# Performance work log

Hardware: AMD Instinct MI355X
Metric: run time of the kernel (lower is better)

## Reference

```python
import jax, jax.numpy as jnp
import numpy as np

EPS_DIST = 1e-10
BN_EPS = 1e-5
K = 3  # nsample / three_nn


def setup_inputs() -> dict:
    key = jax.random.key(0)
    ks = jax.random.split(key, 8)
    B, N, S, D1, D2 = 4, 8192, 2048, 128, 256
    C_in = D1 + D2  # 384
    H = 256
    inp = {
        "pos1": jax.random.normal(ks[0], (B, 3, N), dtype=jnp.float32),
        "pos2": jax.random.normal(ks[1], (B, 3, S), dtype=jnp.float32),
        "feature1": jax.random.normal(ks[2], (B, D1, N), dtype=jnp.float32),
        "feature2": jax.random.normal(ks[3], (B, D2, S), dtype=jnp.float32),
        # MLP layer 1: Conv1d(384->256, k=1) + BN
        "W1": jax.random.normal(ks[4], (H, C_in), dtype=jnp.float32) * (1.0 / np.sqrt(C_in)),
        "b1": jnp.zeros((H,), dtype=jnp.float32),
        "g1": jnp.ones((H,), dtype=jnp.float32),
        "be1": jnp.zeros((H,), dtype=jnp.float32),
        # MLP layer 2: Conv1d(256->256, k=1) + BN
        "W2": jax.random.normal(ks[5], (H, H), dtype=jnp.float32) * (1.0 / np.sqrt(H)),
        "b2": jnp.zeros((H,), dtype=jnp.float32),
        "g2": jnp.ones((H,), dtype=jnp.float32),
        "be2": jnp.zeros((H,), dtype=jnp.float32),
    }
    return inp


def _conv_bn_relu(x, W, b, gamma, beta):
    # x: [B, Cin, N]; 1x1 Conv1d == channel GEMM
    y = jnp.einsum("oc,bcn->bon", W, x) + b[None, :, None]
    # BatchNorm1d in training mode: batch statistics over (B, N)
    mean = jnp.mean(y, axis=(0, 2), keepdims=True)
    var = jnp.mean(jnp.square(y - mean), axis=(0, 2), keepdims=True)
    y = (y - mean) * jax.lax.rsqrt(var + BN_EPS)
    y = y * gamma[None, :, None] + beta[None, :, None]
    return jax.nn.relu(y)


def reference(pos1, pos2, feature1, feature2, W1, b1, g1, be1, W2, b2, g2, be2):
    # pos1: [B,3,N], pos2: [B,3,S], feature1: [B,D1,N], feature2: [B,D2,S]
    p1 = jnp.swapaxes(pos1, 1, 2)  # [B,N,3]
    p2 = jnp.swapaxes(pos2, 1, 2)  # [B,S,3]
    # three_nn: squared-distance 3-NN of each point in p1 among p2
    d2 = (jnp.sum(p1 * p1, -1)[:, :, None]
          + jnp.sum(p2 * p2, -1)[:, None, :]
          - 2.0 * jnp.einsum("bnc,bsc->bns", p1, p2))  # [B,N,S]
    neg_vals, idx = jax.lax.top_k(-d2, K)  # idx: [B,N,3]
    dists = jnp.maximum(-neg_vals, EPS_DIST)  # dists[dists<1e-10]=1e-10
    w = 1.0 / dists
    w = w / jnp.sum(w, -1, keepdims=True)  # [B,N,3]
    # grouping_operation: gather feature2 [B,D,S] by idx -> [B,D,N,3]
    grouped = jax.vmap(lambda f, i: f[:, i])(feature2, idx)
    interpolated = jnp.sum(grouped * w[:, None, :, :], axis=-1)  # [B,D2,N]
    feat = jnp.concatenate([interpolated, feature1], axis=1)  # [B,384,N]
    feat = _conv_bn_relu(feat, W1, b1, g1, be1)
    feat = _conv_bn_relu(feat, W2, b2, g2, be2)
    return feat  # [B,256,N]
```

## Files before the change

### kernel.cpp

```cpp
#include <hip/hip_runtime.h>
#include <hip/hip_bf16.h>
#include <cstdint>

typedef unsigned short u16;
typedef unsigned int u32;
typedef unsigned long long u64;
typedef __bf16 bf16x8 __attribute__((ext_vector_type(8)));
typedef float f32x4 __attribute__((ext_vector_type(4)));
typedef u16 u16x8 __attribute__((ext_vector_type(8)));

__device__ __forceinline__ u16 f2b(float f) {
    unsigned int u = __float_as_uint(f);
    u += 0x7fffu + ((u >> 16) & 1u);
    return (u16)(u >> 16);
}
__device__ __forceinline__ float b2f(u16 h) {
    return __uint_as_float(((unsigned int)h) << 16);
}
__device__ __forceinline__ void async_cp16(void* lds, const void* g) {
    __builtin_amdgcn_global_load_lds((const __attribute__((address_space(1))) void*)g,
                                     (__attribute__((address_space(3))) void*)lds, 16, 0, 0);
}
__device__ __forceinline__ u32 fmono(float f) {
    u32 u = __float_as_uint(f);
    return u ^ (((u32)((int)u >> 31)) | 0x80000000u);
}
__device__ __forceinline__ u64 shfl_xor_u64(u64 v, int mask) {
    u32 lo = (u32)v, hi = (u32)(v >> 32);
    lo = (u32)__shfl_xor((int)lo, mask);
    hi = (u32)__shfl_xor((int)hi, mask);
    return ((u64)hi << 32) | lo;
}
__device__ __forceinline__ void ins3(u64 k, u64& k0, u64& k1, u64& k2) {
    bool c0 = k > k0, c1 = k > k1, c2 = k > k2;
    k2 = c1 ? k1 : (c2 ? k : k2);
    k1 = c0 ? k0 : (c1 ? k : k1);
    k0 = c0 ? k : k0;
}
__device__ __forceinline__ int pkix(int i) { return i + (i >> 6); }

#define NB_NN  1024
#define NB_CVT 160
#define NB_T2  512
#define NB_T1  1024

__global__ __launch_bounds__(256, 8) void prep_kernel(const float* __restrict__ w1,
                                                      const float* __restrict__ w2,
                                                      u16* __restrict__ wb,
                                                      const float* __restrict__ feature2,
                                                      u16* __restrict__ f2t,
                                                      const float* __restrict__ feature1,
                                                      u16* __restrict__ f1t,
                                                      const float* __restrict__ pos1,
                                                      const float* __restrict__ pos2,
                                                      int* __restrict__ idx_out,
                                                      float* __restrict__ w_out) {
    __shared__ __align__(16) char smem[19712];
    int bi = blockIdx.x;
    int tid = threadIdx.x;

    if (bi >= NB_NN) {
        int ci = bi - NB_NN;
        if (ci < NB_CVT) {
            int i = ci * 256 + tid;
            if (i < 40960) {
                const float* src = (i < 24576) ? w1 : w2;
                int k = (i < 24576) ? i : (i - 24576);
                float4 v = *(const float4*)&src[(size_t)k * 4];
                ushort4 o;
                o.x = f2b(v.x); o.y = f2b(v.y); o.z = f2b(v.z); o.w = f2b(v.w);
                *(ushort4*)&wb[(size_t)i * 4] = o;
            }
            return;
        }
        float (*t)[65] = (float (*)[65])smem;
        const float* in; u16* out; int C, S, s0, c0, b;
        if (ci < NB_CVT + NB_T2) {
            int lin = ci - NB_CVT;
            C = 256; S = 2048; in = feature2; out = f2t;
            s0 = (lin & 31) * 64; c0 = ((lin >> 5) & 3) * 64; b = lin >> 7;
        } else {
            int lin = ci - NB_CVT - NB_T2;
            C = 128; S = 8192; in = feature1; out = f1t;
            s0 = (lin & 127) * 64; c0 = ((lin >> 7) & 1) * 64; b = lin >> 8;
        }
        const float* ib = in + (size_t)b * C * S;
        u16* ob = out + (size_t)b * S * C;
        int col = tid & 63, r0 = tid >> 6;
#pragma unroll
        for (int p = 0; p < 16; ++p) {
            int c = p * 4 + r0;
            t[c][col] = ib[(size_t)(c0 + c) * S + s0 + col];
        }
        __syncthreads();
#pragma unroll
        for (int p = 0; p < 16; ++p) {
            int s = p * 4 + r0;
            ob[(size_t)(s0 + s) * C + c0 + col] = f2b(t[col][s]);
        }
        return;
    }

    float4* pk = (float4*)smem;
    u64* warr = (u64*)(smem + 16640);
    int j0 = bi * 32;
    int b = j0 >> 13;
    const float* p2 = pos2 + (size_t)b * 3 * 2048;
    int p = tid & 15, ck = tid >> 4;
    int wv = tid >> 6, lane = tid & 63;
    int na = (j0 & 8191) + p, nbq = na + 16;
    const float* p1 = pos1 + (size_t)b * 3 * 8192;
    float xa = p1[na], ya = p1[8192 + na], za = p1[16384 + na];
    float xb = p1[nbq], yb = p1[8192 + nbq], zb = p1[16384 + nbq];

    u64 a0k = 0, a1k = 0, a2k = 0, b0k = 0, b1k = 0, b2k = 0;

    for (int half = 0; half < 2; ++half) {
        int hbase = half * 1024;
        for (int i = tid; i < 1024; i += 256) {
            int s = hbase + i;
            float x = p2[s], y = p2[2048 + s], z = p2[4096 + s];
            pk[pkix(i)] = make_float4(x, y, z, -0.5f * (x * x + y * y + z * z));
        }
        __syncthreads();

        float ga0 = -3.4e38f, ga1 = -3.4e38f, ga2 = -3.4e38f;
        float gb0 = -3.4e38f, gb1 = -3.4e38f, gb2 = -3.4e38f;
        int ia0 = 0, ia1 = 0, ia2 = 0, ib0 = 0, ib1 = 0, ib2 = 0;
        int sb = ck * 64;
        const float4* pc = pk + pkix(sb);
#pragma unroll 4
        for (int it = 0; it < 64; ++it) {
            float4 cd = pc[it];
            int s = sb + it;
            float ta = fmaf(xa, cd.x, fmaf(ya, cd.y, fmaf(za, cd.z, cd.w)));
            float tb = fmaf(xb, cd.x, fmaf(yb, cd.y, fmaf(zb, cd.z, cd.w)));
            bool a0 = ta > ga0, a1 = ta > ga1, a2 = ta > ga2;
            ga2 = a1 ? ga1 : (a2 ? ta : ga2);
            ia2 = a1 ? ia1 : (a2 ? s : ia2);
            ga1 = a0 ? ga0 : (a1 ? ta : ga1);
            ia1 = a0 ? ia0 : (a1 ? s : ia1);
            ga0 = a0 ? ta : ga0;
            ia0 = a0 ? s : ia0;
            bool b0c = tb > gb0, b1c = tb > gb1, b2c = tb > gb2;
            gb2 = b1c ? gb1 : (b2c ? tb : gb2);
            ib2 = b1c ? ib1 : (b2c ? s : ib2);
            gb1 = b0c ? gb0 : (b1c ? tb : gb1);
            ib1 = b0c ? ib0 : (b1c ? s : ib1);
            gb0 = b0c ? tb : gb0;
            ib0 = b0c ? s : ib0;
        }
        __syncthreads();

        int gi0 = hbase + ia0, gi1 = hbase + ia1, gi2 = hbase + ia2;
        int gj0 = hbase + ib0, gj1 = hbase + ib1, gj2 = hbase + ib2;
        ins3(((u64)fmono(ga0) << 32) | (u64)(2047 - gi0), a0k, a1k, a2k);
        ins3(((u64)fmono(ga1) << 32) | (u64)(2047 - gi1), a0k, a1k, a2k);
        ins3(((u64)fmono(ga2) << 32) | (u64)(2047 - gi2), a0k, a1k, a2k);
        ins3(((u64)fmono(gb0) << 32) | (u64)(2047 - gj0), b0k, b1k, b2k);
        ins3(((u64)fmono(gb1) << 32) | (u64)(2047 - gj1), b0k, b1k, b2k);
        ins3(((u64)fmono(gb2) << 32) | (u64)(2047 - gj2), b0k, b1k, b2k);
    }

#pragma unroll
    for (int mask = 16; mask <= 32; mask <<= 1) {
        u64 pa0 = shfl_xor_u64(a0k, mask), pa1 = shfl_xor_u64(a1k, mask), pa2 = shfl_xor_u64(a2k, mask);
        u64 pb0 = shfl_xor_u64(b0k, mask), pb1 = shfl_xor_u64(b1k, mask), pb2 = shfl_xor_u64(b2k, mask);
        ins3(pa0, a0k, a1k, a2k); ins3(pa1, a0k, a1k, a2k); ins3(pa2, a0k, a1k, a2k);
        ins3(pb0, b0k, b1k, b2k); ins3(pb1, b0k, b1k, b2k); ins3(pb2, b0k, b1k, b2k);
    }
    if (lane < 16) {
        u64* wr = &warr[(wv * 16 + p) * 6];
        wr[0] = a0k; wr[1] = a1k; wr[2] = a2k;
        wr[3] = b0k; wr[4] = b1k; wr[5] = b2k;
    }
    __syncthreads();
    if (tid < 32) {
        int q = tid;
        int pp = q & 15, off = (q < 16) ? 0 : 3;
        const u64* w0 = &warr[pp * 6];
        u64 k0 = w0[off], k1 = w0[off + 1], k2 = w0[off + 2];
#pragma unroll
        for (int w = 1; w < 4; ++w) {
            const u64* wr = &warr[(w * 16 + pp) * 6];
            ins3(wr[off], k0, k1, k2);
            ins3(wr[off + 1], k0, k1, k2);
            ins3(wr[off + 2], k0, k1, k2);
        }
        int s0 = 2047 - (int)(k0 & 0xFFFFFFFFu);
        int s1 = 2047 - (int)(k1 & 0xFFFFFFFFu);
        int s2 = 2047 - (int)(k2 & 0xFFFFFFFFu);
        int j = j0 + q;
        int n = j & 8191;
        float x1 = p1[n], y1 = p1[8192 + n], z1 = p1[16384 + n];
        float n1 = x1 * x1 + y1 * y1 + z1 * z1;
        float X0 = p2[s0], Y0 = p2[2048 + s0], Z0 = p2[4096 + s0];
        float X1 = p2[s1], Y1v = p2[2048 + s1], Z1 = p2[4096 + s1];
        float X2 = p2[s2], Y2v = p2[2048 + s2], Z2 = p2[4096 + s2];
        float t0 = x1 * X0 + y1 * Y0 + z1 * Z0 - 0.5f * (X0 * X0 + Y0 * Y0 + Z0 * Z0);
        float t1 = x1 * X1 + y1 * Y1v + z1 * Z1 - 0.5f * (X1 * X1 + Y1v * Y1v + Z1 * Z1);
        float t2 = x1 * X2 + y1 * Y2v + z1 * Z2 - 0.5f * (X2 * X2 + Y2v * Y2v + Z2 * Z2);
        float d0 = fmaxf(fmaf(-2.f, t0, n1), 1e-10f);
        float d1 = fmaxf(fmaf(-2.f, t1, n1), 1e-10f);
        float d2 = fmaxf(fmaf(-2.f, t2, n1), 1e-10f);
        float w0v = 1.f / d0, w1v = 1.f / d1, w2v = 1.f / d2;
        float inv = 1.f / (w0v + w1v + w2v);
        idx_out[j * 3] = s0; idx_out[j * 3 + 1] = s1; idx_out[j * 3 + 2] = s2;
        w_out[j * 3] = w0v * inv; w_out[j * 3 + 1] = w1v * inv; w_out[j * 3 + 2] = w2v * inv;
    }
}

__global__ __launch_bounds__(256) void gather_kernel(const u16* __restrict__ f2t,
                                                     const int* __restrict__ idx,
                                                     const float* __restrict__ wgt,
                                                     u16* __restrict__ interp) {
    int wv = threadIdx.x >> 6, lane = threadIdx.x & 63;
    int j = blockIdx.x * 4 + wv;
    int b = j >> 13;
    int i0 = idx[j * 3], i1 = idx[j * 3 + 1], i2 = idx[j * 3 + 2];
    float w0 = wgt[j * 3], w1 = wgt[j * 3 + 1], w2 = wgt[j * 3 + 2];
    const u16* r0 = f2t + ((size_t)(b * 2048 + i0)) * 256;
    const u16* r1 = f2t + ((size_t)(b * 2048 + i1)) * 256;
    const u16* r2 = f2t + ((size_t)(b * 2048 + i2)) * 256;
    int c = lane * 4;
    ushort4 v0 = *(const ushort4*)(r0 + c);
    ushort4 v1 = *(const ushort4*)(r1 + c);
    ushort4 v2 = *(const ushort4*)(r2 + c);
    ushort4 o;
    o.x = f2b(w0 * b2f(v0.x) + w1 * b2f(v1.x) + w2 * b2f(v2.x));
    o.y = f2b(w0 * b2f(v0.y) + w1 * b2f(v1.y) + w2 * b2f(v2.y));
    o.z = f2b(w0 * b2f(v0.z) + w1 * b2f(v1.z) + w2 * b2f(v2.z));
    o.w = f2b(w0 * b2f(v0.w) + w1 * b2f(v1.w) + w2 * b2f(v2.w));
    *(ushort4*)(interp + (size_t)j * 256 + c) = o;
}

template <int KT, bool SPLIT, bool FUSE>
__global__ __launch_bounds__(256, 2) void gemm_kernel(const u16* __restrict__ A1,
                                                      const u16* __restrict__ A2,
                                                      const u16* __restrict__ Bw,
                                                      const float* __restrict__ bias,
                                                      const float* __restrict__ stats_in,
                                                      const float* __restrict__ g_in,
                                                      const float* __restrict__ be_in,
                                                      u16* __restrict__ Yb,
                                                      float* __restrict__ stats) {
    __shared__ __align__(16) char smemA[36864];
    u16* Al = (u16*)smemA;
    u16* Bl = (u16*)(smemA + 16384);
    u16* T  = (u16*)smemA;
    float2* BNT = (float2*)(smemA + 34816);
    int tid = threadIdx.x;
    int lane = tid & 63, wv = tid >> 6;
    int j0 = blockIdx.x * 128, m0 = blockIdx.y * 128;
    int l15 = lane & 15, q = lane >> 4;
    int wj = (wv >> 1) * 64, wm = (wv & 1) * 64;
    f32x4 acc[4][4];
#pragma unroll
    for (int i = 0; i < 4; ++i)
#pragma unroll
        for (int jj = 0; jj < 4; ++jj) acc[i][jj] = (f32x4){0.f, 0.f, 0.f, 0.f};

    if (FUSE) {
        int m = tid;
        const float inv = 1.f / 32768.f;
        float mean = stats_in[m] * inv;
        float var = stats_in[256 + m] * inv - mean * mean;
        float a = g_in[m] * rsqrtf(var + 1e-5f);
        BNT[m] = make_float2(a, be_in[m] - mean * a);
        __syncthreads();
    }

    int rbase = wv * 32;
    int lrow = lane >> 3, lchunk = lane & 7;
    const u16* Bg = Bw + (size_t)m0 * KT;

    for (int k0 = 0; k0 < KT; k0 += 64) {
        if (FUSE) {
            int c = k0 + lchunk * 8;
            float2 bn[8];
#pragma unroll
            for (int e = 0; e < 8; ++e) bn[e] = BNT[c + e];
#pragma unroll
            for (int qq = 0; qq < 4; ++qq) {
                int row = rbase + qq * 8;
                u16x8 y = *(const u16x8*)&A1[(size_t)(j0 + row + lrow) * 256 + c];
                u16x8 o;
#pragma unroll
                for (int e = 0; e < 8; ++e)
                    o[e] = f2b(fmaxf(b2f(y[e]) * bn[e].x + bn[e].y, 0.f));
                *(u16x8*)&Al[(row + lrow) * 64 + lchunk * 8] = o;
                async_cp16(&Bl[row * 64], Bg + (size_t)(row + lrow) * KT + k0 + lchunk * 8);
            }
        } else {
            const u16* src; int stride;
            if (!SPLIT || k0 < 256) { src = A1 + (size_t)j0 * 256 + k0; stride = 256; }
            else                    { src = A2 + (size_t)j0 * 128 + (k0 - 256); stride = 128; }
#pragma unroll
            for (int qq = 0; qq < 4; ++qq) {
                int row = rbase + qq * 8;
                async_cp16(&Al[row * 64], src + (size_t)(row + lrow) * stride + lchunk * 8);
                async_cp16(&Bl[row * 64], Bg + (size_t)(row + lrow) * KT + k0 + lchunk * 8);
            }
        }
        __syncthreads();
#pragma unroll
        for (int ks = 0; ks < 2; ++ks) {
            bf16x8 af[4], bfr[4];
#pragma unroll
            for (int i = 0; i < 4; ++i)
                af[i] = *(const bf16x8*)&Al[(wj + i * 16 + l15) * 64 + ks * 32 + q * 8];
#pragma unroll
            for (int i = 0; i < 4; ++i)
                bfr[i] = *(const bf16x8*)&Bl[(wm + i * 16 + l15) * 64 + ks * 32 + q * 8];
#pragma unroll
            for (int i = 0; i < 4; ++i)
#pragma unroll
                for (int jj = 0; jj < 4; ++jj)
                    acc[i][jj] = __builtin_amdgcn_mfma_f32_16x16x32_bf16(af[i], bfr[jj],
                                                                         acc[i][jj], 0, 0, 0);
        }
        __syncthreads();
    }
#pragma unroll
    for (int jj = 0; jj < 4; ++jj) {
        int ml = wm + jj * 16 + l15;
        float bv = bias[m0 + ml];
        float s = 0.f, s2 = 0.f;
#pragma unroll
        for (int i = 0; i < 4; ++i) {
            int jl = wj + i * 16 + q * 4;
#pragma unroll
            for (int r = 0; r < 4; ++r) {
                float v = acc[i][jj][r] + bv;
                s += v; s2 += v * v;
                T[(jl + r) * 136 + ml] = f2b(v);
            }
        }
        s += __shfl_xor(s, 16); s += __shfl_xor(s, 32);
        s2 += __shfl_xor(s2, 16); s2 += __shfl_xor(s2, 32);
        if (q == 0) {
            atomicAdd(&stats[m0 + ml], s);
            atomicAdd(&stats[256 + m0 + ml], s2);
        }
    }
    __syncthreads();
#pragma unroll
    for (int it = 0; it < 8; ++it) {
        int jl = it * 16 + wv * 4 + q;
        u16x8 v = *(const u16x8*)&T[jl * 136 + l15 * 8];
        *(u16x8*)&Yb[(size_t)(j0 + jl) * 256 + m0 + l15 * 8] = v;
    }
}

__global__ __launch_bounds__(256) void final_out_kernel(const u16* __restrict__ Y2,
                                                        const float* __restrict__ stats,
                                                        const float* __restrict__ g,
                                                        const float* __restrict__ be,
                                                        float* __restrict__ out) {
    __shared__ float t[64][65];
    int j0 = blockIdx.x * 64, o0 = blockIdx.y * 64;
    int tid = threadIdx.x;
    int c4 = (tid & 15) * 4, rw = tid >> 4;
#pragma unroll
    for (int p = 0; p < 4; ++p) {
        int jl = p * 16 + rw;
        ushort4 v = *(const ushort4*)&Y2[(size_t)(j0 + jl) * 256 + o0 + c4];
        t[jl][c4] = b2f(v.x); t[jl][c4 + 1] = b2f(v.y);
        t[jl][c4 + 2] = b2f(v.z); t[jl][c4 + 3] = b2f(v.w);
    }
    __syncthreads();
    int b = j0 >> 13, n0 = j0 & 8191;
    const float inv = 1.f / 32768.f;
#pragma unroll
    for (int p = 0; p < 4; ++p) {
        int ol = p * 16 + rw;
        int o = o0 + ol;
        float mean = stats[o] * inv;
        float var = stats[256 + o] * inv - mean * mean;
        float a = g[o] * rsqrtf(var + 1e-5f);
        float s = be[o] - mean * a;
        float4 v;
        v.x = fmaxf(t[c4][ol] * a + s, 0.f);
        v.y = fmaxf(t[c4 + 1][ol] * a + s, 0.f);
        v.z = fmaxf(t[c4 + 2][ol] * a + s, 0.f);
        v.w = fmaxf(t[c4 + 3][ol] * a + s, 0.f);
        *(float4*)&out[(size_t)b * 2097152 + (size_t)o * 8192 + n0 + c4] = v;
    }
}

extern "C" void kernel_launch(void* const* d_in, const int* in_sizes, int n_in,
                              void* d_out, int out_size, void* d_ws, size_t ws_size,
                              hipStream_t stream) {
    const float* pos1 = (const float*)d_in[0];
    const float* pos2 = (const float*)d_in[1];
    const float* feature1 = (const float*)d_in[2];
    const float* feature2 = (const float*)d_in[3];
    const float* W1 = (const float*)d_in[4];
    const float* b1 = (const float*)d_in[5];
    const float* g1 = (const float*)d_in[6];
    const float* be1 = (const float*)d_in[7];
    const float* W2 = (const float*)d_in[8];
    const float* b2 = (const float*)d_in[9];
    const float* g2 = (const float*)d_in[10];
    const float* be2 = (const float*)d_in[11];

    char* ws = (char*)d_ws;
    int*   IDX    = (int*)(ws + 0);
    float* WGT    = (float*)(ws + 393216);
    u16*   W1B    = (u16*)(ws + 786432);
    u16*   W2B    = (u16*)(ws + 983040);
    float* STATS  = (float*)(ws + 1114112);
    u16*   F2T    = (u16*)(ws + 1118208);
    u16*   F1T    = (u16*)(ws + 5312512);
    u16*   INTERP = (u16*)(ws + 13701120);
    u16*   Y1     = (u16*)(ws + 30478336);
    u16*   Y2     = (u16*)(ws + 47255552);
    float* OUT    = (float*)d_out;

    hipMemsetAsync(STATS, 0, 1024 * sizeof(float), stream);
    prep_kernel<<<NB_NN + NB_CVT + NB_T2 + NB_T1, 256, 0, stream>>>(
        W1, W2, W1B, feature2, F2T, feature1, F1T, pos1, pos2, IDX, WGT);
    gather_kernel<<<8192, 256, 0, stream>>>(F2T, IDX, WGT, INTERP);
    gemm_kernel<384, true, false><<<dim3(256, 2), 256, 0, stream>>>(
        INTERP, F1T, W1B, b1, nullptr, nullptr, nullptr, Y1, STATS);
    gemm_kernel<256, false, true><<<dim3(256, 2), 256, 0, stream>>>(
        Y1, nullptr, W2B, b2, STATS, g1, be1, Y2, STATS + 512);
    final_out_kernel<<<dim3(512, 4), 256, 0, stream>>>(Y2, STATS + 512, g2, be2, OUT);
}
```

Measured before the change: 201.9 us.

## Fuse 3-NN interpolation gather into first GEMM and widen NN blocks to 64 queries

Removes the separate gather kernel and the INTERP buffer. The first GEMM now builds its A tile for k<256 by loading the three neighbour rows of F2T, weighting and summing them, and writing the result to LDS directly. This saves a full write and reread of the interpolated activations, but the GEMM's A loads for those k-steps become synchronous and redundant across the two m-blocks. Separately, the three-NN search now handles 64 queries per block (4 per thread) instead of 32, which improves reuse of each pos2 LDS read. The cost is more registers, so launch bounds drop from 8 to 4 blocks.

```diff
diff --git a/kernel.cpp b/kernel.cpp
--- a/kernel.cpp
+++ b/kernel.cpp
@@ -39,12 +39,12 @@
 }
 __device__ __forceinline__ int pkix(int i) { return i + (i >> 6); }
 
-#define NB_NN  1024
+#define NB_NN  512
 #define NB_CVT 160
 #define NB_T2  512
 #define NB_T1  1024
 
-__global__ __launch_bounds__(256, 8) void prep_kernel(const float* __restrict__ w1,
+__global__ __launch_bounds__(256, 4) void prep_kernel(const float* __restrict__ w1,
                                                       const float* __restrict__ w2,
                                                       u16* __restrict__ wb,
                                                       const float* __restrict__ feature2,
@@ -55,7 +55,7 @@
                                                       const float* __restrict__ pos2,
                                                       int* __restrict__ idx_out,
                                                       float* __restrict__ w_out) {
-    __shared__ __align__(16) char smem[19712];
+    __shared__ __align__(16) char smem[22784];
     int bi = blockIdx.x;
     int tid = threadIdx.x;
 
@@ -103,17 +103,21 @@
 
     float4* pk = (float4*)smem;
     u64* warr = (u64*)(smem + 16640);
-    int j0 = bi * 32;
+    int j0 = bi * 64;
     int b = j0 >> 13;
     const float* p2 = pos2 + (size_t)b * 3 * 2048;
     int p = tid & 15, ck = tid >> 4;
     int wv = tid >> 6, lane = tid & 63;
-    int na = (j0 & 8191) + p, nbq = na + 16;
     const float* p1 = pos1 + (size_t)b * 3 * 8192;
-    float xa = p1[na], ya = p1[8192 + na], za = p1[16384 + na];
-    float xb = p1[nbq], yb = p1[8192 + nbq], zb = p1[16384 + nbq];
-
-    u64 a0k = 0, a1k = 0, a2k = 0, b0k = 0, b1k = 0, b2k = 0;
+    float qx[4], qy[4], qz[4];
+#pragma unroll
+    for (int t = 0; t < 4; ++t) {
+        int n = (j0 & 8191) + p + t * 16;
+        qx[t] = p1[n]; qy[t] = p1[8192 + n]; qz[t] = p1[16384 + n];
+    }
+    u64 key[4][3];
+#pragma unroll
+    for (int t = 0; t < 4; ++t) { key[t][0] = 0; key[t][1] = 0; key[t][2] = 0; }
 
     for (int half = 0; half < 2; ++half) {
         int hbase = half * 1024;
@@ -124,73 +128,76 @@
         }
         __syncthreads();
 
-        float ga0 = -3.4e38f, ga1 = -3.4e38f, ga2 = -3.4e38f;
-        float gb0 = -3.4e38f, gb1 = -3.4e38f, gb2 = -3.4e38f;
-        int ia0 = 0, ia1 = 0, ia2 = 0, ib0 = 0, ib1 = 0, ib2 = 0;
+        float g[4][3]; int id[4][3];
+#pragma unroll
+        for (int t = 0; t < 4; ++t) {
+            g[t][0] = -3.4e38f; g[t][1] = -3.4e38f; g[t][2] = -3.4e38f;
+            id[t][0] = 0; id[t][1] = 0; id[t][2] = 0;
+        }
         int sb = ck * 64;
         const float4* pc = pk + pkix(sb);
-#pragma unroll 4
+#pragma unroll 2
         for (int it = 0; it < 64; ++it) {
             float4 cd = pc[it];
             int s = sb + it;
-            float ta = fmaf(xa, cd.x, fmaf(ya, cd.y, fmaf(za, cd.z, cd.w)));
-            float tb = fmaf(xb, cd.x, fmaf(yb, cd.y, fmaf(zb, cd.z, cd.w)));
-            bool a0 = ta > ga0, a1 = ta > ga1, a2 = ta > ga2;
-            ga2 = a1 ? ga1 : (a2 ? ta : ga2);
-            ia2 = a1 ? ia1 : (a2 ? s : ia2);
-            ga1 = a0 ? ga0 : (a1 ? ta : ga1);
-            ia1 = a0 ? ia0 : (a1 ? s : ia1);
-            ga0 = a0 ? ta : ga0;
-            ia0 = a0 ? s : ia0;
-            bool b0c = tb > gb0, b1c = tb > gb1, b2c = tb > gb2;
-            gb2 = b1c ? gb1 : (b2c ? tb : gb2);
-            ib2 = b1c ? ib1 : (b2c ? s : ib2);
-            gb1 = b0c ? gb0 : (b1c ? tb : gb1);
-            ib1 = b0c ? ib0 : (b1c ? s : ib1);
-            gb0 = b0c ? tb : gb0;
-            ib0 = b0c ? s : ib0;
-        }
-        __syncthreads();
-
-        int gi0 = hbase + ia0, gi1 = hbase + ia1, gi2 = hbase + ia2;
-        int gj0 = hbase + ib0, gj1 = hbase + ib1, gj2 = hbase + ib2;
-        ins3(((u64)fmono(ga0) << 32) | (u64)(2047 - gi0), a0k, a1k, a2k);
-        ins3(((u64)fmono(ga1) << 32) | (u64)(2047 - gi1), a0k, a1k, a2k);
-        ins3(((u64)fmono(ga2) << 32) | (u64)(2047 - gi2), a0k, a1k, a2k);
-        ins3(((u64)fmono(gb0) << 32) | (u64)(2047 - gj0), b0k, b1k, b2k);
-        ins3(((u64)fmono(gb1) << 32) | (u64)(2047 - gj1), b0k, b1k, b2k);
-        ins3(((u64)fmono(gb2) << 32) | (u64)(2047 - gj2), b0k, b1k, b2k);
+#pragma unroll
+            for (int t = 0; t < 4; ++t) {
+                float tv = fmaf(qx[t], cd.x, fmaf(qy[t], cd.y, fmaf(qz[t], cd.z, cd.w)));
+                bool c0 = tv > g[t][0], c1 = tv > g[t][1], c2 = tv > g[t][2];
+                g[t][2] = c1 ? g[t][1] : (c2 ? tv : g[t][2]);
+                id[t][2] = c1 ? id[t][1] : (c2 ? s : id[t][2]);
+                g[t][1] = c0 ? g[t][0] : (c1 ? tv : g[t][1]);
+                id[t][1] = c0 ? id[t][0] : (c1 ? s : id[t][1]);
+                g[t][0] = c0 ? tv : g[t][0];
+                id[t][0] = c0 ? s : id[t][0];
+            }
+        }
+        __syncthreads();
+
+#pragma unroll
+        for (int t = 0; t < 4; ++t) {
+#pragma unroll
+            for (int r = 0; r < 3; ++r)
+                ins3(((u64)fmono(g[t][r]) << 32) | (u64)(2047 - (hbase + id[t][r])),
+                     key[t][0], key[t][1], key[t][2]);
+        }
     }
 
 #pragma unroll
     for (int mask = 16; mask <= 32; mask <<= 1) {
-        u64 pa0 = shfl_xor_u64(a0k, mask), pa1 = shfl_xor_u64(a1k, mask), pa2 = shfl_xor_u64(a2k, mask);
-        u64 pb0 = shfl_xor_u64(b0k, mask), pb1 = shfl_xor_u64(b1k, mask), pb2 = shfl_xor_u64(b2k, mask);
-        ins3(pa0, a0k, a1k, a2k); ins3(pa1, a0k, a1k, a2k); ins3(pa2, a0k, a1k, a2k);
-        ins3(pb0, b0k, b1k, b2k); ins3(pb1, b0k, b1k, b2k); ins3(pb2, b0k, b1k, b2k);
+#pragma unroll
+        for (int t = 0; t < 4; ++t) {
+            u64 m0 = shfl_xor_u64(key[t][0], mask);
+            u64 m1 = shfl_xor_u64(key[t][1], mask);
+            u64 m2 = shfl_xor_u64(key[t][2], mask);
+            ins3(m0, key[t][0], key[t][1], key[t][2]);
+            ins3(m1, key[t][0], key[t][1], key[t][2]);
+            ins3(m2, key[t][0], key[t][1], key[t][2]);
+        }
     }
     if (lane < 16) {
-        u64* wr = &warr[(wv * 16 + p) * 6];
-        wr[0] = a0k; wr[1] = a1k; wr[2] = a2k;
-        wr[3] = b0k; wr[4] = b1k; wr[5] = b2k;
+        u64* wr = &warr[(wv * 16 + p) * 12];
+#pragma unroll
+        for (int t = 0; t < 4; ++t) {
+            wr[t * 3 + 0] = key[t][0]; wr[t * 3 + 1] = key[t][1]; wr[t * 3 + 2] = key[t][2];
+        }
     }
     __syncthreads();
-    if (tid < 32) {
-        int q = tid;
-        int pp = q & 15, off = (q < 16) ? 0 : 3;
-        const u64* w0 = &warr[pp * 6];
-        u64 k0 = w0[off], k1 = w0[off + 1], k2 = w0[off + 2];
+    if (tid < 64) {
+        int pp = tid & 15, t = tid >> 4;
+        const u64* w0 = &warr[pp * 12 + t * 3];
+        u64 k0 = w0[0], k1 = w0[1], k2 = w0[2];
 #pragma unroll
         for (int w = 1; w < 4; ++w) {
-            const u64* wr = &warr[(w * 16 + pp) * 6];
-            ins3(wr[off], k0, k1, k2);
-            ins3(wr[off + 1], k0, k1, k2);
-            ins3(wr[off + 2], k0, k1, k2);
+            const u64* wr = &warr[(w * 16 + pp) * 12 + t * 3];
+            ins3(wr[0], k0, k1, k2);
+            ins3(wr[1], k0, k1, k2);
+            ins3(wr[2], k0, k1, k2);
         }
         int s0 = 2047 - (int)(k0 & 0xFFFFFFFFu);
         int s1 = 2047 - (int)(k1 & 0xFFFFFFFFu);
         int s2 = 2047 - (int)(k2 & 0xFFFFFFFFu);
-        int j = j0 + q;
+        int j = j0 + pp + t * 16;
         int n = j & 8191;
         float x1 = p1[n], y1 = p1[8192 + n], z1 = p1[16384 + n];
         float n1 = x1 * x1 + y1 * y1 + z1 * z1;
@@ -210,35 +217,13 @@
     }
 }
 
-__global__ __launch_bounds__(256) void gather_kernel(const u16* __restrict__ f2t,
-                                                     const int* __restrict__ idx,
-                                                     const float* __restrict__ wgt,
-                                                     u16* __restrict__ interp) {
-    int wv = threadIdx.x >> 6, lane = threadIdx.x & 63;
-    int j = blockIdx.x * 4 + wv;
-    int b = j >> 13;
-    int i0 = idx[j * 3], i1 = idx[j * 3 + 1], i2 = idx[j * 3 + 2];
-    float w0 = wgt[j * 3], w1 = wgt[j * 3 + 1], w2 = wgt[j * 3 + 2];
-    const u16* r0 = f2t + ((size_t)(b * 2048 + i0)) * 256;
-    const u16* r1 = f2t + ((size_t)(b * 2048 + i1)) * 256;
-    const u16* r2 = f2t + ((size_t)(b * 2048 + i2)) * 256;
-    int c = lane * 4;
-    ushort4 v0 = *(const ushort4*)(r0 + c);
-    ushort4 v1 = *(const ushort4*)(r1 + c);
-    ushort4 v2 = *(const ushort4*)(r2 + c);
-    ushort4 o;
-    o.x = f2b(w0 * b2f(v0.x) + w1 * b2f(v1.x) + w2 * b2f(v2.x));
-    o.y = f2b(w0 * b2f(v0.y) + w1 * b2f(v1.y) + w2 * b2f(v2.y));
-    o.z = f2b(w0 * b2f(v0.z) + w1 * b2f(v1.z) + w2 * b2f(v2.z));
-    o.w = f2b(w0 * b2f(v0.w) + w1 * b2f(v1.w) + w2 * b2f(v2.w));
-    *(ushort4*)(interp + (size_t)j * 256 + c) = o;
-}
-
-template <int KT, bool SPLIT, bool FUSE>
+template <int KT, bool GATHER, bool FUSE>
 __global__ __launch_bounds__(256, 2) void gemm_kernel(const u16* __restrict__ A1,
                                                       const u16* __restrict__ A2,
                                                       const u16* __restrict__ Bw,
                                                       const float* __restrict__ bias,
+                                                      const int* __restrict__ idx,
+                                                      const float* __restrict__ wgt,
                                                       const float* __restrict__ stats_in,
                                                       const float* __restrict__ g_in,
                                                       const float* __restrict__ be_in,
@@ -260,6 +245,10 @@
 #pragma unroll
         for (int jj = 0; jj < 4; ++jj) acc[i][jj] = (f32x4){0.f, 0.f, 0.f, 0.f};
 
+    int rbase = wv * 32;
+    int lrow = lane >> 3, lchunk = lane & 7;
+    const u16* Bg = Bw + (size_t)m0 * KT;
+
     if (FUSE) {
         int m = tid;
         const float inv = 1.f / 32768.f;
@@ -270,12 +259,39 @@
         __syncthreads();
     }
 
-    int rbase = wv * 32;
-    int lrow = lane >> 3, lchunk = lane & 7;
-    const u16* Bg = Bw + (size_t)m0 * KT;
+    const u16* grow0[4]; const u16* grow1[4]; const u16* grow2[4];
+    float gw0[4], gw1[4], gw2[4];
+    if (GATHER) {
+#pragma unroll
+        for (int qq = 0; qq < 4; ++qq) {
+            int jl = rbase + qq * 8 + lrow;
+            int j = j0 + jl;
+            int bb = j >> 13;
+            const u16* fb = A1 + (size_t)bb * 2048 * 256;
+            grow0[qq] = fb + (size_t)idx[j * 3 + 0] * 256;
+            grow1[qq] = fb + (size_t)idx[j * 3 + 1] * 256;
+            grow2[qq] = fb + (size_t)idx[j * 3 + 2] * 256;
+            gw0[qq] = wgt[j * 3 + 0]; gw1[qq] = wgt[j * 3 + 1]; gw2[qq] = wgt[j * 3 + 2];
+        }
+    }
 
     for (int k0 = 0; k0 < KT; k0 += 64) {
-        if (FUSE) {
+        if (GATHER && k0 < 256) {
+            int c = k0 + lchunk * 8;
+#pragma unroll
+            for (int qq = 0; qq < 4; ++qq) {
+                int row = rbase + qq * 8;
+                u16x8 v0 = *(const u16x8*)(grow0[qq] + c);
+                u16x8 v1 = *(const u16x8*)(grow1[qq] + c);
+                u16x8 v2 = *(const u16x8*)(grow2[qq] + c);
+                u16x8 o;
+#pragma unroll
+                for (int e = 0; e < 8; ++e)
+                    o[e] = f2b(gw0[qq] * b2f(v0[e]) + gw1[qq] * b2f(v1[e]) + gw2[qq] * b2f(v2[e]));
+                *(u16x8*)&Al[(row + lrow) * 64 + lchunk * 8] = o;
+                async_cp16(&Bl[row * 64], Bg + (size_t)(row + lrow) * KT + k0 + lchunk * 8);
+            }
+        } else if (FUSE) {
             int c = k0 + lchunk * 8;
             float2 bn[8];
 #pragma unroll
@@ -292,13 +308,11 @@
                 async_cp16(&Bl[row * 64], Bg + (size_t)(row + lrow) * KT + k0 + lchunk * 8);
             }
         } else {
-            const u16* src; int stride;
-            if (!SPLIT || k0 < 256) { src = A1 + (size_t)j0 * 256 + k0; stride = 256; }
-            else                    { src = A2 + (size_t)j0 * 128 + (k0 - 256); stride = 128; }
+            const u16* src = A2 + (size_t)j0 * 128 + (k0 - 256);
 #pragma unroll
             for (int qq = 0; qq < 4; ++qq) {
                 int row = rbase + qq * 8;
-                async_cp16(&Al[row * 64], src + (size_t)(row + lrow) * stride + lchunk * 8);
+                async_cp16(&Al[row * 64], src + (size_t)(row + lrow) * 128 + lchunk * 8);
                 async_cp16(&Bl[row * 64], Bg + (size_t)(row + lrow) * KT + k0 + lchunk * 8);
             }
         }
@@ -412,18 +426,16 @@
     float* STATS  = (float*)(ws + 1114112);
     u16*   F2T    = (u16*)(ws + 1118208);
     u16*   F1T    = (u16*)(ws + 5312512);
-    u16*   INTERP = (u16*)(ws + 13701120);
-    u16*   Y1     = (u16*)(ws + 30478336);
-    u16*   Y2     = (u16*)(ws + 47255552);
+    u16*   Y1     = (u16*)(ws + 13701120);
+    u16*   Y2     = (u16*)(ws + 30478336);
     float* OUT    = (float*)d_out;
 
     hipMemsetAsync(STATS, 0, 1024 * sizeof(float), stream);
     prep_kernel<<<NB_NN + NB_CVT + NB_T2 + NB_T1, 256, 0, stream>>>(
         W1, W2, W1B, feature2, F2T, feature1, F1T, pos1, pos2, IDX, WGT);
-    gather_kernel<<<8192, 256, 0, stream>>>(F2T, IDX, WGT, INTERP);
     gemm_kernel<384, true, false><<<dim3(256, 2), 256, 0, stream>>>(
-        INTERP, F1T, W1B, b1, nullptr, nullptr, nullptr, Y1, STATS);
+        F2T, F1T, W1B, b1, IDX, WGT, nullptr, nullptr, nullptr, Y1, STATS);
     gemm_kernel<256, false, true><<<dim3(256, 2), 256, 0, stream>>>(
-        Y1, nullptr, W2B, b2, STATS, g1, be1, Y2, STATS + 512);
+        Y1, nullptr, W2B, b2, nullptr, nullptr, STATS, g1, be1, Y2, STATS + 512);
     final_out_kernel<<<dim3(512, 4), 256, 0, stream>>>(Y2, STATS + 512, g2, be2, OUT);
 }
```

Result: no change. 199.3 us (-1.3%).
